# Kernel tuning notes

Hardware: AMD Instinct MI355X
Metric: run time of the kernel (lower is better)

## Reference

```python
import jax, jax.numpy as jnp
import numpy as np

S, B, E, H, V, L = 512, 64, 512, 768, 32000, 32
PAD_WORD, PAD_LABEL = 1, 0
PAD_BIAS = 10000.0


def _linear_init(key, fin, fout):
    # matches torch nn.Linear default U(-1/sqrt(fin), 1/sqrt(fin))
    kw, kb = jax.random.split(key)
    s = 1.0 / np.sqrt(fin)
    W = jax.random.uniform(kw, (fin, fout), minval=-s, maxval=s, dtype=jnp.float32)
    b = jax.random.uniform(kb, (fout,), minval=-s, maxval=s, dtype=jnp.float32)
    return W, b


def setup_inputs() -> dict:
    key = jax.random.key(0)
    ks = jax.random.split(key, 9)
    tokens = jax.random.randint(ks[0], (S, B), 0, V, dtype=jnp.int32)
    tags = jax.random.randint(ks[1], (S, B), 0, L, dtype=jnp.int32)
    embedding = jax.random.normal(ks[2], (V, E), dtype=jnp.float32)
    # gate order along the 4H axis: r, f, g, o (matches the 8 separate Linears, stacked)
    Wi_f, bi_f = _linear_init(ks[3], E, 4 * H)
    Wh_f, bh_f = _linear_init(ks[4], H, 4 * H)
    Wi_b, bi_b = _linear_init(ks[5], E, 4 * H)
    Wh_b, bh_b = _linear_init(ks[6], H, 4 * H)
    Wout, bout = _linear_init(ks[7], 2 * H, L)
    return {"tokens": tokens, "tags": tags, "embedding": embedding,
            "Wi_f": Wi_f, "bi_f": bi_f, "Wh_f": Wh_f, "bh_f": bh_f,
            "Wi_b": Wi_b, "bi_b": bi_b, "Wh_b": Wh_b, "bh_b": bh_b,
            "Wout": Wout, "bout": bout}


def _forward(tokens, embedding, Wi_f, bi_f, Wh_f, bh_f, Wi_b, bi_b, Wh_b, bh_b, Wout, bout):
    emb = embedding[tokens]                      # [S,B,E]
    b = tokens.shape[1]
    h = emb.shape[-1] * 0 + Wh_f.shape[0]
    # ---- forward direction: true LSTM-style recurrence ----
    xf = jnp.einsum('sbe,eg->sbg', emb, Wi_f) + bi_f   # [S,B,4H] precomputed input gates

    def step_f(carry, x):
        hid, c = carry
        g = x + hid @ Wh_f + bh_f
        r, f, gg, o = jnp.split(g, 4, axis=-1)
        c = jax.nn.sigmoid(f) * c + jax.nn.sigmoid(r) * jnp.tanh(gg)
        hid = jax.nn.sigmoid(o) * jnp.tanh(c)
        return (hid, c), hid

    z = jnp.zeros((b, h), dtype=emb.dtype)
    (hT, _), hs_f = jax.lax.scan(step_f, (z, z), xf)   # hs_f: [S,B,H]

    # ---- backward direction: source never updates `hidden`, so the hidden
    # projection uses the CONSTANT final forward hidden hT at every step.
    gb = jnp.einsum('sbe,eg->sbg', emb, Wi_b) + bi_b + hT @ Wh_b + bh_b  # [S,B,4H]
    r2, f2, g2, o2 = jnp.split(gb, 4, axis=-1)
    r2 = jax.nn.sigmoid(r2); f2 = jax.nn.sigmoid(f2)
    g2 = jnp.tanh(g2);       o2 = jax.nn.sigmoid(o2)

    def step_b(c2, gates):
        r, f, g, o = gates
        c2 = f * c2 + r * g
        return c2, o * jnp.tanh(c2)

    _, hs_b = jax.lax.scan(step_b, z, (r2, f2, g2, o2), reverse=True)  # [S,B,H], original order

    outputs = jnp.concatenate([hs_f, hs_b], axis=-1)   # [S,B,2H]
    out = outputs @ Wout + bout                        # [S,B,L]
    pad_mask = (tokens == PAD_WORD).astype(out.dtype)
    out = out.at[:, :, PAD_LABEL].add(pad_mask * PAD_BIAS)
    return out


def reference(tokens, tags, embedding, Wi_f, bi_f, Wh_f, bh_f, Wi_b, bi_b, Wh_b, bh_b, Wout, bout):
    del tags  # unused in forward, kept for signature fidelity
    return _forward(tokens, embedding, Wi_f, bi_f, Wh_f, bh_f, Wi_b, bi_b, Wh_b, bh_b, Wout, bout)
```

## Files before the change

kernel.cpp:

```cpp
#include <hip/hip_runtime.h>
#include <hip/hip_bf16.h>
#include <stdint.h>

typedef __attribute__((ext_vector_type(8))) short bf16x8;
typedef __attribute__((ext_vector_type(4))) float f32x4;
typedef __attribute__((ext_vector_type(4))) unsigned int u32x4;
typedef unsigned long long ull_t;

#define S_LEN 512
#define B_DIM 64
#define E_DIM 512
#define H_DIM 768
#define G4    3072
#define H2    1536
#define M_ROWS 32768
#define CHUNK 128
#define CM    8192
#define SLW   24
#define WPS   8
#define WPR   256
#define RWRD  4096
#define PSTR  16384
#define KRES  640
#define KREG  4
#define WROW  648
#define NTILES 1536
#define EROW  520

__device__ __forceinline__ float sigmf_(float x) { return 1.0f / (1.0f + __expf(-x)); }
__device__ __forceinline__ float tanhf2(float x) {
  x = fminf(fmaxf(x, -20.0f), 20.0f);
  float e = __expf(2.0f * x);
  return (e - 1.0f) / (e + 1.0f);
}
__device__ __forceinline__ float bfu(unsigned short u) { return __uint_as_float((unsigned)u << 16); }
__device__ __forceinline__ unsigned short packbf(float a) {
  __hip_bfloat16 t = __float2bfloat16(a);
  unsigned short b;
  __builtin_memcpy(&b, &t, 2);
  return b;
}

__global__ __launch_bounds__(256) void k_gather(const int* __restrict__ tokens,
                                                const float* __restrict__ emb,
                                                __hip_bfloat16* __restrict__ out) {
  const int t = blockIdx.x * 256 + threadIdx.x;
  const int e0 = t * 8;
  const int row = e0 >> 9;
  const int k = e0 & 511;
  const int tok = tokens[row];
  const float4* p = (const float4*)(emb + (size_t)tok * E_DIM + k);
  const float4 v0 = p[0], v1 = p[1];
  __align__(16) __hip_bfloat16 tmp[8];
  tmp[0] = __float2bfloat16(v0.x); tmp[1] = __float2bfloat16(v0.y);
  tmp[2] = __float2bfloat16(v0.z); tmp[3] = __float2bfloat16(v0.w);
  tmp[4] = __float2bfloat16(v1.x); tmp[5] = __float2bfloat16(v1.y);
  tmp[6] = __float2bfloat16(v1.z); tmp[7] = __float2bfloat16(v1.w);
  *(bf16x8*)(out + (size_t)t * 8) = *(const bf16x8*)tmp;
}

__global__ __launch_bounds__(256) void k_transpose_cast(const float* __restrict__ src,
                                                        __hip_bfloat16* __restrict__ dst,
                                                        int Rs, int Cs) {
  __shared__ float tile[32][33];
  const int tx = threadIdx.x & 31, ty = threadIdx.x >> 5;
  const int c0 = blockIdx.x * 32, r0 = blockIdx.y * 32;
  #pragma unroll
  for (int i = ty; i < 32; i += 8)
    tile[i][tx] = src[(size_t)(r0 + i) * Cs + c0 + tx];
  __syncthreads();
  #pragma unroll
  for (int i = ty; i < 32; i += 8)
    dst[(size_t)(c0 + i) * Rs + r0 + tx] = __float2bfloat16(tile[tx][i]);
}

__global__ __launch_bounds__(256) void k_bias(const float* __restrict__ bi,
                                              const float* __restrict__ bh,
                                              float* __restrict__ bias) {
  const int n = blockIdx.x * 256 + threadIdx.x;
  bias[n] = bi[n] + bh[n];
}

__device__ __forceinline__ void gemm_tile_e(char* pool, int tile,
                                            const __hip_bfloat16* __restrict__ A,
                                            const __hip_bfloat16* __restrict__ BT,
                                            const float* __restrict__ bias,
                                            __hip_bfloat16* __restrict__ C) {
  auto As = (__hip_bfloat16 (*)[40])pool;
  auto Bs = (__hip_bfloat16 (*)[40])(pool + 10240);
  const int tid = threadIdx.x;
  const int wave = tid >> 6, lane = tid & 63;
  const int q = lane >> 4, lr = lane & 15;
  const int wm = (wave >> 1) * 64, wn = (wave & 1) * 64;
  const int nb = tile % 24, mb = tile / 24;
  const int m0 = mb * 128, n0 = nb * 128;
  const int srow = tid >> 2, skseg = (tid & 3) * 8;

  f32x4 acc[4][4];
  #pragma unroll
  for (int i = 0; i < 4; ++i)
    #pragma unroll
    for (int j = 0; j < 4; ++j) { f32x4 z = {0.f, 0.f, 0.f, 0.f}; acc[i][j] = z; }

  for (int kt = 0; kt < 16; ++kt) {
    __syncthreads();
    const int kbase = kt * 32 + skseg;
    *(bf16x8*)&As[srow][skseg]      = *(const bf16x8*)(A + (size_t)(m0 + srow) * E_DIM + kbase);
    *(bf16x8*)&As[srow + 64][skseg] = *(const bf16x8*)(A + (size_t)(m0 + srow + 64) * E_DIM + kbase);
    *(bf16x8*)&Bs[srow][skseg]      = *(const bf16x8*)(BT + (size_t)(n0 + srow) * E_DIM + kbase);
    *(bf16x8*)&Bs[srow + 64][skseg] = *(const bf16x8*)(BT + (size_t)(n0 + srow + 64) * E_DIM + kbase);
    __syncthreads();
    bf16x8 af[4], bfr[4];
    #pragma unroll
    for (int mt = 0; mt < 4; ++mt) af[mt] = *(const bf16x8*)&As[wm + mt * 16 + lr][q * 8];
    #pragma unroll
    for (int nt = 0; nt < 4; ++nt) bfr[nt] = *(const bf16x8*)&Bs[wn + nt * 16 + lr][q * 8];
    #pragma unroll
    for (int mt = 0; mt < 4; ++mt)
      #pragma unroll
      for (int nt = 0; nt < 4; ++nt)
        acc[mt][nt] = __builtin_amdgcn_mfma_f32_16x16x32_bf16(af[mt], bfr[nt], acc[mt][nt], 0, 0, 0);
  }
  #pragma unroll
  for (int mt = 0; mt < 4; ++mt) {
    #pragma unroll
    for (int nt = 0; nt < 4; ++nt) {
      const int col = n0 + wn + nt * 16 + lr;
      const float bv = bias[col];
      #pragma unroll
      for (int i = 0; i < 4; ++i) {
        const int row = m0 + wm + mt * 16 + q * 4 + i;
        C[(size_t)row * G4 + col] = __float2bfloat16(acc[mt][nt][i] + bv);
      }
    }
  }
}

__device__ __forceinline__ void gemm_tile_g(char* pool, int tile,
                                            const int* __restrict__ tokens_c,
                                            const float* __restrict__ emb,
                                            const __hip_bfloat16* __restrict__ BT,
                                            const float* __restrict__ bias,
                                            __hip_bfloat16* __restrict__ C) {
  auto As = (__hip_bfloat16 (*)[40])pool;
  auto Bs = (__hip_bfloat16 (*)[40])(pool + 10240);
  const int tid = threadIdx.x;
  const int wave = tid >> 6, lane = tid & 63;
  const int q = lane >> 4, lr = lane & 15;
  const int wm = (wave >> 1) * 64, wn = (wave & 1) * 64;
  const int nb = tile % 24, mb = tile / 24;
  const int m0 = mb * 128, n0 = nb * 128;
  const int srow = tid >> 2, skseg = (tid & 3) * 8;
  const int tok0 = tokens_c[m0 + srow];
  const int tok1 = tokens_c[m0 + srow + 64];

  f32x4 acc[4][4];
  #pragma unroll
  for (int i = 0; i < 4; ++i)
    #pragma unroll
    for (int j = 0; j < 4; ++j) { f32x4 z = {0.f, 0.f, 0.f, 0.f}; acc[i][j] = z; }

  for (int kt = 0; kt < 16; ++kt) {
    __syncthreads();
    const int kbase = kt * 32 + skseg;
    {
      const float* ap = emb + (size_t)tok0 * E_DIM + kbase;
      const float4 v0 = *(const float4*)ap, v1 = *(const float4*)(ap + 4);
      __align__(16) __hip_bfloat16 t8[8];
      t8[0] = __float2bfloat16(v0.x); t8[1] = __float2bfloat16(v0.y);
      t8[2] = __float2bfloat16(v0.z); t8[3] = __float2bfloat16(v0.w);
      t8[4] = __float2bfloat16(v1.x); t8[5] = __float2bfloat16(v1.y);
      t8[6] = __float2bfloat16(v1.z); t8[7] = __float2bfloat16(v1.w);
      *(bf16x8*)&As[srow][skseg] = *(const bf16x8*)t8;
    }
    {
      const float* ap = emb + (size_t)tok1 * E_DIM + kbase;
      const float4 v0 = *(const float4*)ap, v1 = *(const float4*)(ap + 4);
      __align__(16) __hip_bfloat16 t8[8];
      t8[0] = __float2bfloat16(v0.x); t8[1] = __float2bfloat16(v0.y);
      t8[2] = __float2bfloat16(v0.z); t8[3] = __float2bfloat16(v0.w);
      t8[4] = __float2bfloat16(v1.x); t8[5] = __float2bfloat16(v1.y);
      t8[6] = __float2bfloat16(v1.z); t8[7] = __float2bfloat16(v1.w);
      *(bf16x8*)&As[srow + 64][skseg] = *(const bf16x8*)t8;
    }
    *(bf16x8*)&Bs[srow][skseg]      = *(const bf16x8*)(BT + (size_t)(n0 + srow) * E_DIM + kbase);
    *(bf16x8*)&Bs[srow + 64][skseg] = *(const bf16x8*)(BT + (size_t)(n0 + srow + 64) * E_DIM + kbase);
    __syncthreads();
    bf16x8 af[4], bfr[4];
    #pragma unroll
    for (int mt = 0; mt < 4; ++mt) af[mt] = *(const bf16x8*)&As[wm + mt * 16 + lr][q * 8];
    #pragma unroll
    for (int nt = 0; nt < 4; ++nt) bfr[nt] = *(const bf16x8*)&Bs[wn + nt * 16 + lr][q * 8];
    #pragma unroll
    for (int mt = 0; mt < 4; ++mt)
      #pragma unroll
      for (int nt = 0; nt < 4; ++nt)
        acc[mt][nt] = __builtin_amdgcn_mfma_f32_16x16x32_bf16(af[mt], bfr[nt], acc[mt][nt], 0, 0, 0);
  }
  #pragma unroll
  for (int mt = 0; mt < 4; ++mt) {
    #pragma unroll
    for (int nt = 0; nt < 4; ++nt) {
      const int col = n0 + wn + nt * 16 + lr;
      const float bv = bias[col];
      #pragma unroll
      for (int i = 0; i < 4; ++i) {
        const int row = m0 + wm + mt * 16 + q * 4 + i;
        C[(size_t)row * G4 + col] = __float2bfloat16(acc[mt][nt][i] + bv);
      }
    }
  }
}

__global__ __launch_bounds__(256) void k_gemm_e(const __hip_bfloat16* __restrict__ A,
                                                const __hip_bfloat16* __restrict__ BT,
                                                const float* __restrict__ bias,
                                                __hip_bfloat16* __restrict__ C) {
  __shared__ __align__(16) char pool[20480];
  gemm_tile_e(pool, blockIdx.x, A, BT, bias, C);
}
__global__ __launch_bounds__(256) void k_gemm_g(const int* __restrict__ tokens_c,
                                                const float* __restrict__ emb,
                                                const __hip_bfloat16* __restrict__ BT,
                                                const float* __restrict__ bias,
                                                __hip_bfloat16* __restrict__ C) {
  __shared__ __align__(16) char pool[20480];
  gemm_tile_g(pool, blockIdx.x, tokens_c, emb, BT, bias, C);
}

__device__ __forceinline__ void out_block8(char* pool, int ob,
                                           const __hip_bfloat16* __restrict__ Hs,
                                           const float* __restrict__ Wout,
                                           const float* __restrict__ bout,
                                           const int* __restrict__ tokens,
                                           float* __restrict__ out) {
  auto rowbuf = (float (*)[1536])pool;
  const int r0 = ob * 8;
  const int tid = threadIdx.x;
  for (int idx = tid; idx < 8 * 1536; idx += 256) {
    const int rr = idx / 1536, k = idx % 1536;
    rowbuf[rr][k] = __bfloat162float(Hs[(size_t)(r0 + rr) * H2 + k]);
  }
  __syncthreads();
  const int l = tid & 31, rr = tid >> 5;
  float acc = bout[l];
  #pragma unroll 8
  for (int k = 0; k < 1536; ++k) acc += rowbuf[rr][k] * Wout[k * 32 + l];
  const int row = r0 + rr;
  if (l == 0 && tokens[row] == 1) acc += 10000.0f;
  out[(size_t)row * 32 + l] = acc;
  __syncthreads();
}

__global__ __launch_bounds__(256) void k_out(const __hip_bfloat16* __restrict__ Hs,
                                             const float* __restrict__ Wout,
                                             const float* __restrict__ bout,
                                             const int* __restrict__ tokens,
                                             float* __restrict__ out) {
  __shared__ __align__(16) char pool[49152];
  out_block8(pool, blockIdx.x, Hs, Wout, bout, tokens, out);
}

__global__ __launch_bounds__(256, 1) void k_fwd_fused(const __hip_bfloat16* __restrict__ X,
                                                      const __hip_bfloat16* __restrict__ WhTf,
                                                      ull_t* __restrict__ hbuf,
                                                      __hip_bfloat16* __restrict__ Hs,
                                                      float* __restrict__ cstate,
                                                      float* __restrict__ hT,
                                                      int chunk,
                                                      const __hip_bfloat16* __restrict__ EmbA,
                                                      const int* __restrict__ tokens_nx,
                                                      const float* __restrict__ emb,
                                                      const __hip_bfloat16* __restrict__ WiT_nx,
                                                      const float* __restrict__ Bias_nx,
                                                      __hip_bfloat16* __restrict__ Xw) {
  __shared__ __align__(16) char pool[155904];
  const int bx = blockIdx.x;

  if (bx >= 128) {
    const int nw = gridDim.x - 128;
    if (EmbA) {
      for (int t = bx - 128; t < NTILES; t += nw)
        gemm_tile_e(pool, t, EmbA, WiT_nx, Bias_nx, Xw);
    } else {
      for (int t = bx - 128; t < NTILES; t += nw)
        gemm_tile_g(pool, t, tokens_nx, emb, WiT_nx, Bias_nx, Xw);
    }
    return;
  }

  unsigned short* wlds = (unsigned short*)pool;
  auto h_stage = (unsigned short (*)[776])(pool + 124416);
  auto g_lds   = (float (*)[16][26])(pool + 149248);

  const int group = bx >> 5;
  const int slice = bx & 31;
  const int r0 = group * 16;
  const int j0 = slice * SLW;
  const int tid = threadIdx.x;
  const int w = tid >> 6;
  const int lane = tid & 63;
  const int q = lane >> 4, lr = lane & 15;
  const int base = chunk * CHUNK;

  const int prow = tid >> 4;
  const int pw   = tid & 15;

  const int row  = tid >> 3;
  const int wloc = tid & 7;
  const int col0 = 3 * wloc;

  for (int c = tid; c < 96 * (KRES / 8); c += 256) {
    const int r = c / (KRES / 8), k8 = c % (KRES / 8);
    const int gate = r / SLW, n = r % SLW;
    const float4 v = *(const float4*)(WhTf + (size_t)(gate * H_DIM + j0 + n) * H_DIM + k8 * 8);
    *(float4*)(wlds + (size_t)r * WROW + k8 * 8) = v;
  }

  const int wn0 = lr;
  const int wn1 = 16 + (lr & 7);
  bf16x8 wr0[KREG], wr1[KREG];
  #pragma unroll
  for (int kk = 0; kk < KREG; ++kk) {
    const int ko = KRES + kk * 32 + q * 8;
    wr0[kk] = *(const bf16x8*)(WhTf + (size_t)(w * H_DIM + j0 + wn0) * H_DIM + ko);
    wr1[kk] = *(const bf16x8*)(WhTf + (size_t)(w * H_DIM + j0 + wn1) * H_DIM + ko);
  }

  float cr[3] = {0.f, 0.f, 0.f};
  if (tid < 128) {
    const float* cs = cstate + (size_t)(r0 + row) * H_DIM + j0 + col0;
    cr[0] = cs[0]; cr[1] = cs[1]; cr[2] = cs[2];
  }

  const unsigned skipbit = ((pw >> 2) == (slice & 3)) ? (1u << (slice >> 2)) : 0u;

  __syncthreads();

  for (int s = 0; s < CHUNK; ++s) {
    const int gs = base + s;

    unsigned short xs[4][3];
    if (tid < 128) {
      const unsigned short* xp = (const unsigned short*)(X + ((size_t)s * B_DIM + r0 + row) * G4 + j0 + col0);
      #pragma unroll
      for (int g = 0; g < 4; ++g)
        #pragma unroll
        for (int j = 0; j < 3; ++j) xs[g][j] = xp[g * H_DIM + j];
    }

    const ull_t* hc = hbuf + ((size_t)(gs & 1)) * PSTR + (size_t)group * RWRD
                    + (size_t)prow * WPR + 2 * pw;
    u32x4 d0 = {0,0,0,0}, d1 = {0,0,0,0}, d2 = {0,0,0,0}, d3 = {0,0,0,0};
    u32x4 d4 = {0,0,0,0}, d5 = {0,0,0,0}, d6 = {0,0,0,0}, d7 = {0,0,0,0};
    const unsigned pollmask = (s == 0) ? 0xFFu : (0xFFu ^ skipbit);
    {
      const unsigned e16 = (unsigned)(unsigned short)gs;
      unsigned need = pollmask;
      long guard = 0;
      for (;;) {
#define POLL_LD(i, dv) \
        if (need & (1u << (i))) \
          asm volatile("global_load_dwordx4 %0, %1, off sc0 sc1" \
                       : "=v"(dv) : "v"(hc + 32 * (i)) : "memory");
        POLL_LD(0, d0) POLL_LD(1, d1) POLL_LD(2, d2) POLL_LD(3, d3)
        POLL_LD(4, d4) POLL_LD(5, d5) POLL_LD(6, d6) POLL_LD(7, d7)
#undef POLL_LD
        asm volatile("s_waitcnt vmcnt(0)"
                     : "+v"(d0), "+v"(d1), "+v"(d2), "+v"(d3),
                       "+v"(d4), "+v"(d5), "+v"(d6), "+v"(d7)
                     :: "memory");
        unsigned nn = 0;
#define POLL_CK(i, dv) \
        if ((need & (1u << (i))) && \
            ((((dv).x & 0xFFFFu) != e16) || (((dv).z & 0xFFFFu) != e16))) nn |= 1u << (i);
        POLL_CK(0, d0) POLL_CK(1, d1) POLL_CK(2, d2) POLL_CK(3, d3)
        POLL_CK(4, d4) POLL_CK(5, d5) POLL_CK(6, d6) POLL_CK(7, d7)
#undef POLL_CK
        need = nn;
        if (!need) break;
        if (++guard > (1L << 20)) break;
        __builtin_amdgcn_s_sleep(1);
      }
    }
    {
#define STAGE_PAIR(i, dv) \
      if (pollmask & (1u << (i))) { \
        unsigned* hp = (unsigned*)&h_stage[prow][6 * pw + 96 * (i)]; \
        hp[0] = ((dv).x >> 16) | ((dv).y << 16); \
        hp[1] = ((dv).y >> 16) | ((dv).z & 0xFFFF0000u); \
        hp[2] = (dv).w; \
      }
      STAGE_PAIR(0, d0) STAGE_PAIR(1, d1) STAGE_PAIR(2, d2) STAGE_PAIR(3, d3)
      STAGE_PAIR(4, d4) STAGE_PAIR(5, d5) STAGE_PAIR(6, d6) STAGE_PAIR(7, d7)
#undef STAGE_PAIR
    }
    __syncthreads();

    f32x4 acc0 = {0.f, 0.f, 0.f, 0.f};
    f32x4 acc1 = {0.f, 0.f, 0.f, 0.f};
    {
      const unsigned short* wb = wlds + (size_t)w * SLW * WROW;
      #pragma unroll
      for (int kt = 0; kt < KRES / 32; ++kt) {
        const int ko = kt * 32 + q * 8;
        const bf16x8 a  = *(const bf16x8*)&h_stage[lr][ko];
        const bf16x8 b0 = *(const bf16x8*)(wb + (size_t)wn0 * WROW + ko);
        const bf16x8 b1 = *(const bf16x8*)(wb + (size_t)wn1 * WROW + ko);
        acc0 = __builtin_amdgcn_mfma_f32_16x16x32_bf16(a, b0, acc0, 0, 0, 0);
        acc1 = __builtin_amdgcn_mfma_f32_16x16x32_bf16(a, b1, acc1, 0, 0, 0);
      }
      #pragma unroll
      for (int kk = 0; kk < KREG; ++kk) {
        const bf16x8 a = *(const bf16x8*)&h_stage[lr][KRES + kk * 32 + q * 8];
        acc0 = __builtin_amdgcn_mfma_f32_16x16x32_bf16(a, wr0[kk], acc0, 0, 0, 0);
        acc1 = __builtin_amdgcn_mfma_f32_16x16x32_bf16(a, wr1[kk], acc1, 0, 0, 0);
      }
    }
    #pragma unroll
    for (int i = 0; i < 4; ++i) g_lds[w][q * 4 + i][lr] = acc0[i];
    if (lr < 8) {
      #pragma unroll
      for (int i = 0; i < 4; ++i) g_lds[w][q * 4 + i][16 + lr] = acc1[i];
    }
    __syncthreads();

    if (tid < 128) {
      float h[3];
      #pragma unroll
      for (int j = 0; j < 3; ++j) {
        const float rv = g_lds[0][row][col0 + j] + bfu(xs[0][j]);
        const float fv = g_lds[1][row][col0 + j] + bfu(xs[1][j]);
        const float gv = g_lds[2][row][col0 + j] + bfu(xs[2][j]);
        const float ov = g_lds[3][row][col0 + j] + bfu(xs[3][j]);
        const float c = sigmf_(fv) * cr[j] + sigmf_(rv) * tanhf2(gv);
        cr[j] = c;
        h[j] = sigmf_(ov) * tanhf2(c);
      }
      const unsigned short b0 = packbf(h[0]), b1 = packbf(h[1]), b2 = packbf(h[2]);
      const ull_t wv = (ull_t)(unsigned short)(gs + 1)
                     | ((ull_t)b0 << 16) | ((ull_t)b1 << 32) | ((ull_t)b2 << 48);
      __hip_atomic_store(hbuf + ((size_t)((gs + 1) & 1)) * PSTR + (size_t)group * RWRD
                         + (size_t)row * WPR + slice * WPS + wloc,
                         wv, __ATOMIC_RELAXED, __HIP_MEMORY_SCOPE_AGENT);
      h_stage[row][j0 + col0]     = b0;
      h_stage[row][j0 + col0 + 1] = b1;
      h_stage[row][j0 + col0 + 2] = b2;
      unsigned short* hsp = (unsigned short*)(Hs + ((size_t)gs * B_DIM + r0 + row) * H2 + j0 + col0);
      hsp[0] = b0; hsp[1] = b1; hsp[2] = b2;
      if (chunk == 3 && s == CHUNK - 1) {
        float* hp = hT + (size_t)(r0 + row) * H_DIM + j0 + col0;
        hp[0] = h[0]; hp[1] = h[1]; hp[2] = h[2];
      }
    }
  }

  if (tid < 128) {
    float* cs = cstate + (size_t)(r0 + row) * H_DIM + j0 + col0;
    cs[0] = cr[0]; cs[1] = cr[1]; cs[2] = cr[2];
  }
}

__global__ __launch_bounds__(256) void k_hTW(const float* __restrict__ hT,
                                             const float* __restrict__ Whb,
                                             float* __restrict__ hTW) {
  const int b = blockIdx.y;
  const int n = blockIdx.x * 256 + threadIdx.x;
  __shared__ float hs[768];
  for (int i = threadIdx.x; i < 768; i += 256) hs[i] = hT[b * 768 + i];
  __syncthreads();
  float acc = 0.f;
  #pragma unroll 4
  for (int k = 0; k < 768; ++k) acc += hs[k] * Whb[(size_t)k * G4 + n];
  hTW[(size_t)b * G4 + n] = acc;
}

__global__ __launch_bounds__(256, 1) void k_bwd_fused2(const __hip_bfloat16* __restrict__ Emb,
                                                       const __hip_bfloat16* __restrict__ WiTb,
                                                       const float* __restrict__ BiasB,
                                                       const float* __restrict__ hTW,
                                                       __hip_bfloat16* __restrict__ Hs,
                                                       float* __restrict__ c2state,
                                                       int chunk, int out_chunk,
                                                       const float* __restrict__ Wout,
                                                       const float* __restrict__ bout,
                                                       const int* __restrict__ tokens,
                                                       float* __restrict__ out) {
  __shared__ __align__(16) char pool[146432];
  const int bx = blockIdx.x;

  if (bx >= 128) {
    if (out_chunk >= 0)
      for (int ob = bx - 128; ob < 1024; ob += 128)
        out_block8(pool, out_chunk * 1024 + ob, Hs, Wout, bout, tokens, out);
    return;
  }

  unsigned short* wlds = (unsigned short*)pool;
  auto emb_s = (unsigned short (*)[EROW])(pool + 99840);
  auto g_lds = (float (*)[2][16][26])(pool + 133120);

  const int group = bx >> 5;
  const int slice = bx & 31;
  const int r0 = group * 16;
  const int j0 = slice * SLW;
  const int tid = threadIdx.x;
  const int w = tid >> 6;
  const int lane = tid & 63;
  const int q = lane >> 4, lr = lane & 15;
  const int base = chunk * CHUNK;

  for (int c = tid; c < 96 * 64; c += 256) {
    const int r = c >> 6, k8 = c & 63;
    const int gate = r / SLW, n = r % SLW;
    *(float4*)(wlds + (size_t)r * EROW + k8 * 8) =
        *(const float4*)(WiTb + (size_t)(gate * H_DIM + j0 + n) * E_DIM + k8 * 8);
  }

  const int row = tid >> 3, wloc = tid & 7, col0 = 3 * wloc;
  float hw0[3], hw1[3], hw2[3], hw3[3], c2r[3] = {0.f, 0.f, 0.f};
  if (tid < 128) {
    const int b = r0 + row;
    #pragma unroll
    for (int j = 0; j < 3; ++j) {
      const int n = j0 + col0 + j;
      hw0[j] = BiasB[n]        + hTW[(size_t)b * G4 + n];
      hw1[j] = BiasB[768 + n]  + hTW[(size_t)b * G4 + 768 + n];
      hw2[j] = BiasB[1536 + n] + hTW[(size_t)b * G4 + 1536 + n];
      hw3[j] = BiasB[2304 + n] + hTW[(size_t)b * G4 + 2304 + n];
      c2r[j] = c2state[(size_t)b * H_DIM + n];
    }
  }
  const int wn0 = lr;
  const int wn1 = 16 + (lr & 7);
  const unsigned short* wb0 = wlds + (size_t)(w * SLW + wn0) * EROW;
  const unsigned short* wb1 = wlds + (size_t)(w * SLW + wn1) * EROW;
  __syncthreads();

  for (int t = CHUNK / 2 - 1; t >= 0; --t) {
    for (int c = tid; c < 32 * 64; c += 256) {
      const int a = c >> 6, k8 = c & 63;
      const int ss = 2 * t + 1 - (a >> 4);
      *(float4*)(&emb_s[a][k8 * 8]) =
          *(const float4*)(Emb + ((size_t)(base + ss) * B_DIM + r0 + (a & 15)) * E_DIM + k8 * 8);
    }
    __syncthreads();

    f32x4 a00 = {0.f,0.f,0.f,0.f}, a01 = {0.f,0.f,0.f,0.f};
    f32x4 a10 = {0.f,0.f,0.f,0.f}, a11 = {0.f,0.f,0.f,0.f};
    #pragma unroll
    for (int kt = 0; kt < 16; ++kt) {
      const int ko = kt * 32 + q * 8;
      const bf16x8 b0 = *(const bf16x8*)(wb0 + ko);
      const bf16x8 b1 = *(const bf16x8*)(wb1 + ko);
      const bf16x8 aA = *(const bf16x8*)(&emb_s[lr][ko]);
      const bf16x8 aB = *(const bf16x8*)(&emb_s[16 + lr][ko]);
      a00 = __builtin_amdgcn_mfma_f32_16x16x32_bf16(aA, b0, a00, 0, 0, 0);
      a01 = __builtin_amdgcn_mfma_f32_16x16x32_bf16(aA, b1, a01, 0, 0, 0);
      a10 = __builtin_amdgcn_mfma_f32_16x16x32_bf16(aB, b0, a10, 0, 0, 0);
      a11 = __builtin_amdgcn_mfma_f32_16x16x32_bf16(aB, b1, a11, 0, 0, 0);
    }
    #pragma unroll
    for (int i = 0; i < 4; ++i) {
      g_lds[w][0][q * 4 + i][lr] = a00[i];
      g_lds[w][1][q * 4 + i][lr] = a10[i];
    }
    if (lr < 8) {
      #pragma unroll
      for (int i = 0; i < 4; ++i) {
        g_lds[w][0][q * 4 + i][16 + lr] = a01[i];
        g_lds[w][1][q * 4 + i][16 + lr] = a11[i];
      }
    }
    __syncthreads();

    if (tid < 128) {
      #pragma unroll
      for (int st = 0; st < 2; ++st) {
        const int gs = base + 2 * t + 1 - st;
        unsigned short hb[3];
        #pragma unroll
        for (int j = 0; j < 3; ++j) {
          const float rv = sigmf_(g_lds[0][st][row][col0 + j] + hw0[j]);
          const float fv = sigmf_(g_lds[1][st][row][col0 + j] + hw1[j]);
          const float gv = tanhf2(g_lds[2][st][row][col0 + j] + hw2[j]);
          const float ov = sigmf_(g_lds[3][st][row][col0 + j] + hw3[j]);
          c2r[j] = fv * c2r[j] + rv * gv;
          hb[j] = packbf(ov * tanhf2(c2r[j]));
        }
        unsigned short* hsp = (unsigned short*)(Hs + ((size_t)gs * B_DIM + r0 + row) * H2
                                                + H_DIM + j0 + col0);
        hsp[0] = hb[0]; hsp[1] = hb[1]; hsp[2] = hb[2];
      }
    }
  }

  if (tid < 128) {
    #pragma unroll
    for (int j = 0; j < 3; ++j)
      c2state[(size_t)(r0 + row) * H_DIM + j0 + col0 + j] = c2r[j];
  }
}

__global__ __launch_bounds__(256) void k_bwd_scan(const __hip_bfloat16* __restrict__ X,
                                                  const float* __restrict__ hTW,
                                                  __hip_bfloat16* __restrict__ Hs,
                                                  float* __restrict__ c2state,
                                                  int chunk) {
  const int t = blockIdx.x * 256 + threadIdx.x;
  const int b = t / H_DIM;
  const int j = t % H_DIM;
  const int base = chunk * CHUNK;
  const float hw0 = hTW[(size_t)b * G4 + j];
  const float hw1 = hTW[(size_t)b * G4 + 768 + j];
  const float hw2 = hTW[(size_t)b * G4 + 1536 + j];
  const float hw3 = hTW[(size_t)b * G4 + 2304 + j];
  float c2 = c2state[t];
  for (int s = CHUNK - 1; s >= 0; --s) {
    const size_t xb = ((size_t)s * B_DIM + b) * G4 + j;
    const float r = sigmf_(__bfloat162float(X[xb]) + hw0);
    const float f = sigmf_(__bfloat162float(X[xb + 768]) + hw1);
    const float g = tanhf2(__bfloat162float(X[xb + 1536]) + hw2);
    const float o = sigmf_(__bfloat162float(X[xb + 2304]) + hw3);
    c2 = f * c2 + r * g;
    Hs[((size_t)(base + s) * B_DIM + b) * H2 + H_DIM + j] = __float2bfloat16(o * tanhf2(c2));
  }
  c2state[t] = c2;
}

extern "C" void kernel_launch(void* const* d_in, const int* in_sizes, int n_in,
                              void* d_out, int out_size, void* d_ws, size_t ws_size,
                              hipStream_t stream) {
  const int*   tokens = (const int*)d_in[0];
  const float* emb    = (const float*)d_in[2];
  const float* Wi_f   = (const float*)d_in[3];
  const float* bi_f   = (const float*)d_in[4];
  const float* Wh_f   = (const float*)d_in[5];
  const float* bh_f   = (const float*)d_in[6];
  const float* Wi_b   = (const float*)d_in[7];
  const float* bi_b   = (const float*)d_in[8];
  const float* Wh_b   = (const float*)d_in[9];
  const float* bh_b   = (const float*)d_in[10];
  const float* Wout   = (const float*)d_in[11];
  const float* bout   = (const float*)d_in[12];
  float* out = (float*)d_out;
  char* ws = (char*)d_ws;

  size_t off = 0;
  auto alloc = [&](size_t bytes) { size_t o = off; off += (bytes + 255) & ~(size_t)255; return o; };
  const size_t oHs    = alloc((size_t)M_ROWS * H2 * 2);
  const size_t oX0    = alloc((size_t)CM * G4 * 2);
  const size_t oWhTf  = alloc((size_t)G4 * H_DIM * 2);
  const size_t oWiTf  = alloc((size_t)G4 * E_DIM * 2);
  const size_t oWiTb  = alloc((size_t)G4 * E_DIM * 2);
  const size_t oBiasF = alloc((size_t)G4 * 4);
  const size_t oBiasB = alloc((size_t)G4 * 4);
  const size_t oHbuf  = alloc((size_t)2 * PSTR * 8);
  const size_t oCst   = alloc((size_t)B_DIM * H_DIM * 4);
  const size_t oHT    = alloc((size_t)B_DIM * H_DIM * 4);
  const size_t oHTW   = alloc((size_t)B_DIM * G4 * 4);
  const size_t oC2    = alloc((size_t)B_DIM * H_DIM * 4);
  const size_t oX1    = alloc((size_t)CM * G4 * 2);
  const bool overlap = (off <= ws_size);
  const size_t oEmb   = alloc((size_t)M_ROWS * E_DIM * 2);
  const bool tierA = (off <= ws_size);
  (void)in_sizes; (void)n_in; (void)out_size;

  __hip_bfloat16* Hs   = (__hip_bfloat16*)(ws + oHs);
  __hip_bfloat16* X0   = (__hip_bfloat16*)(ws + oX0);
  __hip_bfloat16* X1   = overlap ? (__hip_bfloat16*)(ws + oX1) : X0;
  __hip_bfloat16* Emb  = tierA ? (__hip_bfloat16*)(ws + oEmb) : (__hip_bfloat16*)nullptr;
  __hip_bfloat16* WhTf = (__hip_bfloat16*)(ws + oWhTf);
  __hip_bfloat16* WiTf = (__hip_bfloat16*)(ws + oWiTf);
  __hip_bfloat16* WiTb = (__hip_bfloat16*)(ws + oWiTb);
  float*          BiasF= (float*)(ws + oBiasF);
  float*          BiasB= (float*)(ws + oBiasB);
  ull_t*          Hbuf = (ull_t*)(ws + oHbuf);
  float*          Cst  = (float*)(ws + oCst);
  float*          HT   = (float*)(ws + oHT);
  float*          HTW  = (float*)(ws + oHTW);
  float*          C2   = (float*)(ws + oC2);

  hipMemsetAsync(ws + oHbuf, 0, (size_t)2 * PSTR * 8, stream);
  hipMemsetAsync(ws + oCst, 0, (size_t)B_DIM * H_DIM * 4, stream);
  hipMemsetAsync(ws + oC2, 0, (size_t)B_DIM * H_DIM * 4, stream);

  if (tierA)
    k_gather<<<8192, 256, 0, stream>>>(tokens, emb, Emb);
  k_transpose_cast<<<dim3(96, 24), 256, 0, stream>>>(Wh_f, WhTf, 768, 3072);
  k_transpose_cast<<<dim3(96, 16), 256, 0, stream>>>(Wi_f, WiTf, 512, 3072);
  k_transpose_cast<<<dim3(96, 16), 256, 0, stream>>>(Wi_b, WiTb, 512, 3072);
  k_bias<<<12, 256, 0, stream>>>(bi_f, bh_f, BiasF);
  k_bias<<<12, 256, 0, stream>>>(bi_b, bh_b, BiasB);

  if (overlap && tierA) {
    k_gemm_e<<<NTILES, 256, 0, stream>>>(Emb, WiTf, BiasF, X0);
    auto EA = [&](int c) { return Emb + (size_t)c * CM * E_DIM; };
    k_fwd_fused<<<240, 256, 0, stream>>>(X0, WhTf, Hbuf, Hs, Cst, HT, 0,
                                         EA(1), tokens, emb, WiTf, BiasF, X1);
    k_fwd_fused<<<240, 256, 0, stream>>>(X1, WhTf, Hbuf, Hs, Cst, HT, 1,
                                         EA(2), tokens, emb, WiTf, BiasF, X0);
    k_fwd_fused<<<240, 256, 0, stream>>>(X0, WhTf, Hbuf, Hs, Cst, HT, 2,
                                         EA(3), tokens, emb, WiTf, BiasF, X1);
    k_fwd_fused<<<128, 256, 0, stream>>>(X1, WhTf, Hbuf, Hs, Cst, HT, 3,
                                         EA(0), tokens, emb, WiTf, BiasF, X0);
    k_hTW<<<dim3(12, 64), 256, 0, stream>>>(HT, Wh_b, HTW);
    k_bwd_fused2<<<256, 256, 0, stream>>>(Emb, WiTb, BiasB, HTW, Hs, C2, 3, -1,
                                          Wout, bout, tokens, out);
    k_bwd_fused2<<<256, 256, 0, stream>>>(Emb, WiTb, BiasB, HTW, Hs, C2, 2, 3,
                                          Wout, bout, tokens, out);
    k_bwd_fused2<<<256, 256, 0, stream>>>(Emb, WiTb, BiasB, HTW, Hs, C2, 1, 2,
                                          Wout, bout, tokens, out);
    k_bwd_fused2<<<256, 256, 0, stream>>>(Emb, WiTb, BiasB, HTW, Hs, C2, 0, 1,
                                          Wout, bout, tokens, out);
    k_out<<<1024, 256, 0, stream>>>(Hs, Wout, bout, tokens, out);
  } else if (overlap) {
    k_gemm_g<<<NTILES, 256, 0, stream>>>(tokens, emb, WiTf, BiasF, X0);
    k_fwd_fused<<<240, 256, 0, stream>>>(X0, WhTf, Hbuf, Hs, Cst, HT, 0,
                                         nullptr, tokens + 1 * CM, emb, WiTf, BiasF, X1);
    k_fwd_fused<<<240, 256, 0, stream>>>(X1, WhTf, Hbuf, Hs, Cst, HT, 1,
                                         nullptr, tokens + 2 * CM, emb, WiTf, BiasF, X0);
    k_fwd_fused<<<240, 256, 0, stream>>>(X0, WhTf, Hbuf, Hs, Cst, HT, 2,
                                         nullptr, tokens + 3 * CM, emb, WiTf, BiasF, X1);
    k_fwd_fused<<<240, 256, 0, stream>>>(X1, WhTf, Hbuf, Hs, Cst, HT, 3,
                                         nullptr, tokens + 3 * CM, emb, WiTb, BiasB, X0);
    k_hTW<<<dim3(12, 64), 256, 0, stream>>>(HT, Wh_b, HTW);
    k_bwd_scan<<<192, 256, 0, stream>>>(X0, HTW, Hs, C2, 3);
    for (int c = 2; c >= 0; --c) {
      k_gemm_g<<<NTILES, 256, 0, stream>>>(tokens + (size_t)c * CM, emb, WiTb, BiasB, X1);
      k_bwd_scan<<<192, 256, 0, stream>>>(X1, HTW, Hs, C2, c);
    }
    k_out<<<4096, 256, 0, stream>>>(Hs, Wout, bout, tokens, out);
  } else {
    for (int c = 0; c < 4; ++c) {
      k_gemm_g<<<NTILES, 256, 0, stream>>>(tokens + (size_t)c * CM, emb, WiTf, BiasF, X0);
      k_fwd_fused<<<128, 256, 0, stream>>>(X0, WhTf, Hbuf, Hs, Cst, HT, c,
                                           nullptr, tokens, emb, WiTf, BiasF, X0);
    }
    k_hTW<<<dim3(12, 64), 256, 0, stream>>>(HT, Wh_b, HTW);
    for (int c = 3; c >= 0; --c) {
      k_gemm_g<<<NTILES, 256, 0, stream>>>(tokens + (size_t)c * CM, emb, WiTb, BiasB, X0);
      k_bwd_scan<<<192, 256, 0, stream>>>(X0, HTW, Hs, C2, c);
    }
    k_out<<<4096, 256, 0, stream>>>(Hs, Wout, bout, tokens, out);
  }
}
```

Baseline: 3.594 ms.

## Split backward scan over 256 blocks of 8 rows with prefetched embedding double-buffer

Measured after the change: 3.135 ms. -12.8%, faster.

```diff
diff --git a/kernel.cpp b/kernel.cpp
--- a/kernel.cpp
+++ b/kernel.cpp
@@ -475,34 +475,21 @@
   hTW[(size_t)b * G4 + n] = acc;
 }
 
-__global__ __launch_bounds__(256, 1) void k_bwd_fused2(const __hip_bfloat16* __restrict__ Emb,
+__global__ __launch_bounds__(256, 1) void k_bwd_fused3(const __hip_bfloat16* __restrict__ Emb,
                                                        const __hip_bfloat16* __restrict__ WiTb,
                                                        const float* __restrict__ BiasB,
                                                        const float* __restrict__ hTW,
                                                        __hip_bfloat16* __restrict__ Hs,
                                                        float* __restrict__ c2state,
-                                                       int chunk, int out_chunk,
-                                                       const float* __restrict__ Wout,
-                                                       const float* __restrict__ bout,
-                                                       const int* __restrict__ tokens,
-                                                       float* __restrict__ out) {
-  __shared__ __align__(16) char pool[146432];
+                                                       int chunk) {
+  __shared__ __align__(16) unsigned short wlds[96 * EROW];
+  __shared__ __align__(16) unsigned short emb_s[2][16][EROW];
+  __shared__ float g_lds[4][16][26];
+
   const int bx = blockIdx.x;
-
-  if (bx >= 128) {
-    if (out_chunk >= 0)
-      for (int ob = bx - 128; ob < 1024; ob += 128)
-        out_block8(pool, out_chunk * 1024 + ob, Hs, Wout, bout, tokens, out);
-    return;
-  }
-
-  unsigned short* wlds = (unsigned short*)pool;
-  auto emb_s = (unsigned short (*)[EROW])(pool + 99840);
-  auto g_lds = (float (*)[2][16][26])(pool + 133120);
-
   const int group = bx >> 5;
   const int slice = bx & 31;
-  const int r0 = group * 16;
+  const int r0 = group * 8;
   const int j0 = slice * SLW;
   const int tid = threadIdx.x;
   const int w = tid >> 6;
@@ -517,10 +504,10 @@
         *(const float4*)(WiTb + (size_t)(gate * H_DIM + j0 + n) * E_DIM + k8 * 8);
   }
 
-  const int row = tid >> 3, wloc = tid & 7, col0 = 3 * wloc;
+  const int rr = tid >> 3, wloc = tid & 7, col0 = 3 * wloc;
   float hw0[3], hw1[3], hw2[3], hw3[3], c2r[3] = {0.f, 0.f, 0.f};
-  if (tid < 128) {
-    const int b = r0 + row;
+  if (tid < 64) {
+    const int b = r0 + rr;
     #pragma unroll
     for (int j = 0; j < 3; ++j) {
       const int n = j0 + col0 + j;
@@ -535,70 +522,76 @@
   const int wn1 = 16 + (lr & 7);
   const unsigned short* wb0 = wlds + (size_t)(w * SLW + wn0) * EROW;
   const unsigned short* wb1 = wlds + (size_t)(w * SLW + wn1) * EROW;
-  __syncthreads();
-
+
+  int aa[4], kk8[4];
+  #pragma unroll
+  for (int i = 0; i < 4; ++i) { aa[i] = (tid + 256 * i) >> 6; kk8[i] = (tid + 256 * i) & 63; }
+
+  bf16x8 pf0, pf1, pf2, pf3;
+#define PF_LOAD(t) { \
+    pf0 = *(const bf16x8*)(Emb + ((size_t)(base + 2*(t)+1-(aa[0]>>3)) * B_DIM + r0 + (aa[0]&7)) * E_DIM + kk8[0]*8); \
+    pf1 = *(const bf16x8*)(Emb + ((size_t)(base + 2*(t)+1-(aa[1]>>3)) * B_DIM + r0 + (aa[1]&7)) * E_DIM + kk8[1]*8); \
+    pf2 = *(const bf16x8*)(Emb + ((size_t)(base + 2*(t)+1-(aa[2]>>3)) * B_DIM + r0 + (aa[2]&7)) * E_DIM + kk8[2]*8); \
+    pf3 = *(const bf16x8*)(Emb + ((size_t)(base + 2*(t)+1-(aa[3]>>3)) * B_DIM + r0 + (aa[3]&7)) * E_DIM + kk8[3]*8); }
+
+  PF_LOAD(CHUNK / 2 - 1);
+
+  int buf = 0;
   for (int t = CHUNK / 2 - 1; t >= 0; --t) {
-    for (int c = tid; c < 32 * 64; c += 256) {
-      const int a = c >> 6, k8 = c & 63;
-      const int ss = 2 * t + 1 - (a >> 4);
-      *(float4*)(&emb_s[a][k8 * 8]) =
-          *(const float4*)(Emb + ((size_t)(base + ss) * B_DIM + r0 + (a & 15)) * E_DIM + k8 * 8);
-    }
+    *(bf16x8*)&emb_s[buf][aa[0]][kk8[0] * 8] = pf0;
+    *(bf16x8*)&emb_s[buf][aa[1]][kk8[1] * 8] = pf1;
+    *(bf16x8*)&emb_s[buf][aa[2]][kk8[2] * 8] = pf2;
+    *(bf16x8*)&emb_s[buf][aa[3]][kk8[3] * 8] = pf3;
+    if (t > 0) PF_LOAD(t - 1);
     __syncthreads();
 
-    f32x4 a00 = {0.f,0.f,0.f,0.f}, a01 = {0.f,0.f,0.f,0.f};
-    f32x4 a10 = {0.f,0.f,0.f,0.f}, a11 = {0.f,0.f,0.f,0.f};
+    f32x4 a0 = {0.f, 0.f, 0.f, 0.f};
+    f32x4 a1 = {0.f, 0.f, 0.f, 0.f};
     #pragma unroll
     for (int kt = 0; kt < 16; ++kt) {
       const int ko = kt * 32 + q * 8;
+      const bf16x8 av = *(const bf16x8*)&emb_s[buf][lr][ko];
       const bf16x8 b0 = *(const bf16x8*)(wb0 + ko);
       const bf16x8 b1 = *(const bf16x8*)(wb1 + ko);
-      const bf16x8 aA = *(const bf16x8*)(&emb_s[lr][ko]);
-      const bf16x8 aB = *(const bf16x8*)(&emb_s[16 + lr][ko]);
-      a00 = __builtin_amdgcn_mfma_f32_16x16x32_bf16(aA, b0, a00, 0, 0, 0);
-      a01 = __builtin_amdgcn_mfma_f32_16x16x32_bf16(aA, b1, a01, 0, 0, 0);
-      a10 = __builtin_amdgcn_mfma_f32_16x16x32_bf16(aB, b0, a10, 0, 0, 0);
-      a11 = __builtin_amdgcn_mfma_f32_16x16x32_bf16(aB, b1, a11, 0, 0, 0);
-    }
-    #pragma unroll
-    for (int i = 0; i < 4; ++i) {
-      g_lds[w][0][q * 4 + i][lr] = a00[i];
-      g_lds[w][1][q * 4 + i][lr] = a10[i];
-    }
+      a0 = __builtin_amdgcn_mfma_f32_16x16x32_bf16(av, b0, a0, 0, 0, 0);
+      a1 = __builtin_amdgcn_mfma_f32_16x16x32_bf16(av, b1, a1, 0, 0, 0);
+    }
+    #pragma unroll
+    for (int i = 0; i < 4; ++i) g_lds[w][q * 4 + i][lr] = a0[i];
     if (lr < 8) {
       #pragma unroll
-      for (int i = 0; i < 4; ++i) {
-        g_lds[w][0][q * 4 + i][16 + lr] = a01[i];
-        g_lds[w][1][q * 4 + i][16 + lr] = a11[i];
-      }
+      for (int i = 0; i < 4; ++i) g_lds[w][q * 4 + i][16 + lr] = a1[i];
     }
     __syncthreads();
 
-    if (tid < 128) {
+    if (tid < 64) {
       #pragma unroll
       for (int st = 0; st < 2; ++st) {
         const int gs = base + 2 * t + 1 - st;
+        const int m = st * 8 + rr;
         unsigned short hb[3];
         #pragma unroll
         for (int j = 0; j < 3; ++j) {
-          const float rv = sigmf_(g_lds[0][st][row][col0 + j] + hw0[j]);
-          const float fv = sigmf_(g_lds[1][st][row][col0 + j] + hw1[j]);
-          const float gv = tanhf2(g_lds[2][st][row][col0 + j] + hw2[j]);
-          const float ov = sigmf_(g_lds[3][st][row][col0 + j] + hw3[j]);
+          const float rv = sigmf_(g_lds[0][m][col0 + j] + hw0[j]);
+          const float fv = sigmf_(g_lds[1][m][col0 + j] + hw1[j]);
+          const float gv = tanhf2(g_lds[2][m][col0 + j] + hw2[j]);
+          const float ov = sigmf_(g_lds[3][m][col0 + j] + hw3[j]);
           c2r[j] = fv * c2r[j] + rv * gv;
           hb[j] = packbf(ov * tanhf2(c2r[j]));
         }
-        unsigned short* hsp = (unsigned short*)(Hs + ((size_t)gs * B_DIM + r0 + row) * H2
+        unsigned short* hsp = (unsigned short*)(Hs + ((size_t)gs * B_DIM + r0 + rr) * H2
                                                 + H_DIM + j0 + col0);
         hsp[0] = hb[0]; hsp[1] = hb[1]; hsp[2] = hb[2];
       }
     }
-  }
-
-  if (tid < 128) {
+    buf ^= 1;
+  }
+#undef PF_LOAD
+
+  if (tid < 64) {
     #pragma unroll
     for (int j = 0; j < 3; ++j)
-      c2state[(size_t)(r0 + row) * H_DIM + j0 + col0 + j] = c2r[j];
+      c2state[(size_t)(r0 + rr) * H_DIM + j0 + col0 + j] = c2r[j];
   }
 }
 
@@ -705,15 +698,11 @@
     k_fwd_fused<<<128, 256, 0, stream>>>(X1, WhTf, Hbuf, Hs, Cst, HT, 3,
                                          EA(0), tokens, emb, WiTf, BiasF, X0);
     k_hTW<<<dim3(12, 64), 256, 0, stream>>>(HT, Wh_b, HTW);
-    k_bwd_fused2<<<256, 256, 0, stream>>>(Emb, WiTb, BiasB, HTW, Hs, C2, 3, -1,
-                                          Wout, bout, tokens, out);
-    k_bwd_fused2<<<256, 256, 0, stream>>>(Emb, WiTb, BiasB, HTW, Hs, C2, 2, 3,
-                                          Wout, bout, tokens, out);
-    k_bwd_fused2<<<256, 256, 0, stream>>>(Emb, WiTb, BiasB, HTW, Hs, C2, 1, 2,
-                                          Wout, bout, tokens, out);
-    k_bwd_fused2<<<256, 256, 0, stream>>>(Emb, WiTb, BiasB, HTW, Hs, C2, 0, 1,
-                                          Wout, bout, tokens, out);
-    k_out<<<1024, 256, 0, stream>>>(Hs, Wout, bout, tokens, out);
+    k_bwd_fused3<<<256, 256, 0, stream>>>(Emb, WiTb, BiasB, HTW, Hs, C2, 3);
+    k_bwd_fused3<<<256, 256, 0, stream>>>(Emb, WiTb, BiasB, HTW, Hs, C2, 2);
+    k_bwd_fused3<<<256, 256, 0, stream>>>(Emb, WiTb, BiasB, HTW, Hs, C2, 1);
+    k_bwd_fused3<<<256, 256, 0, stream>>>(Emb, WiTb, BiasB, HTW, Hs, C2, 0);
+    k_out<<<4096, 256, 0, stream>>>(Hs, Wout, bout, tokens, out);
   } else if (overlap) {
     k_gemm_g<<<NTILES, 256, 0, stream>>>(tokens, emb, WiTf, BiasF, X0);
     k_fwd_fused<<<240, 256, 0, stream>>>(X0, WhTf, Hbuf, Hs, Cst, HT, 0,
```
